# Performance work log

Measured on AMD Instinct MI355X. Metric: run time of the kernel, lower is better.

Reference implementation:

```python
import jax, jax.numpy as jnp
import numpy as np

N_NODES = 100000
N_EDGES = 1200000
IN_DIM = 256
HID = 64


def _spmm(rows, cols, vals, M):
    # sparse (COO) @ dense: gather source rows, scale by edge vals, scatter-add to dest
    gathered = M[cols] * vals[:, None]          # [E, d]
    return jax.ops.segment_sum(gathered, rows, num_segments=N_NODES)


def _gcn_embed(rows, cols, vals, X, W1, b1, W2, b2):
    # layer 1: SELU(A @ (X W1) + b1)
    Z = _spmm(rows, cols, vals, X @ W1) + b1
    Z = jax.nn.selu(Z)
    # layer 2: A @ (Z W2) + b2 (no activation)
    Z = _spmm(rows, cols, vals, Z @ W2) + b2
    # row-wise L2 normalize (F.normalize, p=2, dim=1)
    norm = jnp.sqrt(jnp.sum(Z * Z, axis=1, keepdims=True))
    return Z / jnp.maximum(norm, 1e-12)


def setup_inputs() -> dict:
    key = jax.random.key(0)
    ks = jax.random.split(key, 10)
    X1 = jax.random.normal(ks[0], (N_NODES, IN_DIM), dtype=jnp.float32)
    X2 = jax.random.normal(ks[1], (N_NODES, IN_DIM), dtype=jnp.float32)
    rows1 = jax.random.randint(ks[2], (N_EDGES,), 0, N_NODES, dtype=jnp.int32)
    cols1 = jax.random.randint(ks[3], (N_EDGES,), 0, N_NODES, dtype=jnp.int32)
    vals1 = jax.random.uniform(ks[4], (N_EDGES,), dtype=jnp.float32)
    rows2 = jax.random.randint(ks[5], (N_EDGES,), 0, N_NODES, dtype=jnp.int32)
    cols2 = jax.random.randint(ks[6], (N_EDGES,), 0, N_NODES, dtype=jnp.int32)
    vals2 = jax.random.uniform(ks[7], (N_EDGES,), dtype=jnp.float32)
    # Xavier-uniform weights, zero biases (reset_parameters)
    lim1 = float(np.sqrt(6.0 / (IN_DIM + HID)))
    lim2 = float(np.sqrt(6.0 / (HID + HID)))
    W1 = jax.random.uniform(ks[8], (IN_DIM, HID), dtype=jnp.float32, minval=-lim1, maxval=lim1)
    W2 = jax.random.uniform(ks[9], (HID, HID), dtype=jnp.float32, minval=-lim2, maxval=lim2)
    b1 = jnp.zeros((HID,), dtype=jnp.float32)
    b2 = jnp.zeros((HID,), dtype=jnp.float32)
    return {"X1": X1, "X2": X2, "rows1": rows1, "cols1": cols1, "vals1": vals1,
            "rows2": rows2, "cols2": cols2, "vals2": vals2,
            "W1": W1, "b1": b1, "W2": W2, "b2": b2}


def reference(X1, X2, rows1, cols1, vals1, rows2, cols2, vals2, W1, b1, W2, b2):
    Z1 = _gcn_embed(rows1, cols1, vals1, X1, W1, b1, W2, b2)
    Z2 = _gcn_embed(rows2, cols2, vals2, X2, W1, b1, W2, b2)
    return (Z1, Z2)
```

## Files before the change

### kernel.cpp

```cpp
#include <hip/hip_runtime.h>
#include <hip/hip_bf16.h>


#define RPB 512
#define EPB 4096
#define MAXB 8192

typedef __attribute__((ext_vector_type(8))) short short8;
typedef __attribute__((ext_vector_type(4))) short short4v;
typedef __attribute__((ext_vector_type(4))) float f32x4;

__device__ __forceinline__ float selu_f(float x) {
    const float scale = 1.0507009873554805f;
    const float alpha = 1.6732632423543772f;
    return x > 0.0f ? scale * x : scale * alpha * (__expf(x) - 1.0f);
}

__device__ __forceinline__ short f2bf(float x) {
    unsigned u = __float_as_uint(x);
    u += 0x7FFF + ((u >> 16) & 1);
    return (short)(u >> 16);
}
__device__ __forceinline__ float bf2f(short h) {
    return __uint_as_float(((unsigned)(unsigned short)h) << 16);
}

__global__ void scan_a(const int* __restrict__ countsB, int* __restrict__ offsB,
                       int* __restrict__ partialsB, int N) {
    const int* counts = countsB + (size_t)blockIdx.y * N;
    int* offs = offsB + (size_t)blockIdx.y * (N + 1);
    int* partials = partialsB + (size_t)blockIdx.y * 512;
    __shared__ int sh[256];
    int tid = threadIdx.x;
    int base = blockIdx.x * 1024 + tid * 4;
    int4 c = make_int4(0, 0, 0, 0);
    if (base + 3 < N) {
        c = *(const int4*)(counts + base);
    } else {
        if (base + 0 < N) c.x = counts[base + 0];
        if (base + 1 < N) c.y = counts[base + 1];
        if (base + 2 < N) c.z = counts[base + 2];
        if (base + 3 < N) c.w = counts[base + 3];
    }
    int tsum = c.x + c.y + c.z + c.w;
    sh[tid] = tsum;
    __syncthreads();
    int val = tsum;
    for (int d = 1; d < 256; d <<= 1) {
        int t = (tid >= d) ? sh[tid - d] : 0;
        __syncthreads();
        val += t;
        sh[tid] = val;
        __syncthreads();
    }
    int excl = val - tsum;
    int4 o;
    o.x = excl; o.y = o.x + c.x; o.z = o.y + c.y; o.w = o.z + c.z;
    if (base + 3 < N) {
        *(int4*)(offs + base) = o;
    } else {
        if (base + 0 < N) offs[base + 0] = o.x;
        if (base + 1 < N) offs[base + 1] = o.y;
        if (base + 2 < N) offs[base + 2] = o.z;
        if (base + 3 < N) offs[base + 3] = o.w;
    }
    if (tid == 255) partials[blockIdx.x] = val;
}

__global__ void scan_b(int* __restrict__ partialsB, int nb) {
    int* partials = partialsB + (size_t)blockIdx.y * 512;
    __shared__ int sh[128];
    int tid = threadIdx.x;
    int v = (tid < nb) ? partials[tid] : 0;
    sh[tid] = v;
    __syncthreads();
    int val = v;
    for (int d = 1; d < 128; d <<= 1) {
        int t = (tid >= d) ? sh[tid - d] : 0;
        __syncthreads();
        val += t;
        sh[tid] = val;
        __syncthreads();
    }
    if (tid < nb) partials[tid] = val - v;
}

__global__ void scan_c(int* __restrict__ offsB, const int* __restrict__ partialsB,
                       int N, int E) {
    int* offs = offsB + (size_t)blockIdx.y * (N + 1);
    const int* partials = partialsB + (size_t)blockIdx.y * 512;
    int tid = threadIdx.x;
    int base = blockIdx.x * 1024 + tid * 4;
    int add = partials[blockIdx.x];
    if (base + 3 < N) {
        int4 o = *(int4*)(offs + base);
        o.x += add; o.y += add; o.z += add; o.w += add;
        *(int4*)(offs + base) = o;
    } else {
        for (int t = 0; t < 4; t++)
            if (base + t < N) offs[base + t] += add;
    }
    if (blockIdx.x == 0 && tid == 0) offs[N] = E;
}

__global__ __launch_bounds__(256) void bucket_hist(const int* __restrict__ r0,
                                                   const int* __restrict__ r1,
                                                   int* __restrict__ cntTB,
                                                   int E, int nbA, int NB, int M) {
    const int* rows = blockIdx.y ? r1 : r0;
    int* cntT = cntTB + (size_t)blockIdx.y * M;
    __shared__ int cnt[256];
    int tid = threadIdx.x;
    cnt[tid] = 0;
    __syncthreads();
    int e0 = blockIdx.x * EPB;
#pragma unroll
    for (int k = 0; k < EPB / 256; k++) {
        int e = e0 + k * 256 + tid;
        if (e < E) atomicAdd(&cnt[rows[e] >> 9], 1);
    }
    __syncthreads();
    if (tid < NB) cntT[tid * nbA + blockIdx.x] = cnt[tid];
}

__global__ __launch_bounds__(256) void coarse_scatter(const int* __restrict__ r0,
                                                      const int* __restrict__ r1,
                                                      const int* __restrict__ c0,
                                                      const int* __restrict__ c1,
                                                      const float* __restrict__ v0,
                                                      const float* __restrict__ v1,
                                                      const int* __restrict__ csOffsB,
                                                      int2* __restrict__ ecvAB,
                                                      int E, int nbA, int NB, int M) {
    const int* rows = blockIdx.y ? r1 : r0;
    const int* cols = blockIdx.y ? c1 : c0;
    const float* vals = blockIdx.y ? v1 : v0;
    const int* csOffs = csOffsB + (size_t)blockIdx.y * (M + 1);
    int2* ecvA = ecvAB + (size_t)blockIdx.y * E;
    __shared__ int cnt[256];
    __shared__ int loc[256];
    __shared__ int gof[256];
    __shared__ int dstBase[EPB];
    __shared__ int2 eLDS[EPB];
    int tid = threadIdx.x, blk = blockIdx.x;
    int e0 = blk * EPB;
    cnt[tid] = 0;
    __syncthreads();
#pragma unroll
    for (int k = 0; k < EPB / 256; k++) {
        int e = e0 + k * 256 + tid;
        if (e < E) atomicAdd(&cnt[rows[e] >> 9], 1);
    }
    __syncthreads();
    int my = cnt[tid];
    loc[tid] = my;
    __syncthreads();
    int val = my;
    for (int d = 1; d < 256; d <<= 1) {
        int t = (tid >= d) ? loc[tid - d] : 0;
        __syncthreads();
        val += t;
        loc[tid] = val;
        __syncthreads();
    }
    int excl = val - my;
    loc[tid] = excl;
    cnt[tid] = excl;
    gof[tid] = (tid < NB) ? csOffs[tid * nbA + blk] : 0;
    __syncthreads();
#pragma unroll
    for (int k = 0; k < EPB / 256; k++) {
        int e = e0 + k * 256 + tid;
        if (e < E) {
            int r = rows[e];
            int b = r >> 9;
            int p = atomicAdd(&cnt[b], 1);
            eLDS[p] = make_int2(((r & (RPB - 1)) << 17) | cols[e],
                                __float_as_int(vals[e]));
            dstBase[p] = gof[b] - loc[b];
        }
    }
    __syncthreads();
    int nE = min(EPB, E - e0);
    for (int j = tid; j < nE; j += 256)
        ecvA[dstBase[j] + j] = eLDS[j];
}

__global__ __launch_bounds__(256) void fine_sort(const int* __restrict__ csOffsB,
                                                 const int2* __restrict__ ecvAB,
                                                 int2* __restrict__ ecvB,
                                                 int* __restrict__ offsB,
                                                 int nbA, int N, int E, int M) {
    const int* csOffs = csOffsB + (size_t)blockIdx.y * (M + 1);
    const int2* ecvA = ecvAB + (size_t)blockIdx.y * E;
    int2* ecv = ecvB + (size_t)blockIdx.y * E;
    int* offs = offsB + (size_t)blockIdx.y * (N + 1);
    __shared__ int rcnt[RPB], roff[RPB], rcur[RPB];
    __shared__ int sh[256];
    __shared__ int2 eLDS[MAXB];
    int b = blockIdx.x, tid = threadIdx.x;
    int bs = csOffs[b * nbA];
    int be = csOffs[(b + 1) * nbA];
    int cntE = be - bs;
    if (cntE > MAXB) cntE = MAXB;
    rcnt[tid] = 0;
    rcnt[tid + 256] = 0;
    __syncthreads();
    for (int j = tid; j < cntE; j += 256)
        atomicAdd(&rcnt[ecvA[bs + j].x >> 17], 1);
    __syncthreads();
    int a0 = rcnt[2 * tid], a1 = rcnt[2 * tid + 1];
    int ps = a0 + a1;
    sh[tid] = ps;
    __syncthreads();
    int val = ps;
    for (int d = 1; d < 256; d <<= 1) {
        int t = (tid >= d) ? sh[tid - d] : 0;
        __syncthreads();
        val += t;
        sh[tid] = val;
        __syncthreads();
    }
    int exclPair = val - ps;
    roff[2 * tid] = exclPair;
    roff[2 * tid + 1] = exclPair + a0;
    rcur[2 * tid] = exclPair;
    rcur[2 * tid + 1] = exclPair + a0;
    __syncthreads();
    int row0 = b * RPB;
    for (int t2 = tid; t2 < RPB; t2 += 256) {
        int row = row0 + t2;
        if (row <= N) offs[row] = bs + roff[t2];
    }
    if (b == 0 && tid == 0) offs[N] = E;
    for (int j = tid; j < cntE; j += 256) {
        int2 p = ecvA[bs + j];
        int pos = atomicAdd(&rcur[p.x >> 17], 1);
        if (pos < MAXB) eLDS[pos] = make_int2(p.x & 0x1FFFF, p.y);
    }
    __syncthreads();
    for (int j = tid; j < cntE; j += 256)
        ecv[bs + j] = eLDS[j];
}

__global__ void prep_w2(const float* __restrict__ W1, short* __restrict__ th1,
                        short* __restrict__ tl1,
                        const float* __restrict__ W2, short* __restrict__ th2,
                        short* __restrict__ tl2) {
    int idx = blockIdx.x * 256 + threadIdx.x;
    const int n1 = 256 * 64;
    if (idx < n1) {
        int k = idx >> 6, n = idx & 63;
        float x = W1[idx];
        short h = f2bf(x);
        short l = f2bf(x - bf2f(h));
        th1[n * 256 + k] = h;
        tl1[n * 256 + k] = l;
    } else if (idx - n1 < 64 * 64) {
        int i2 = idx - n1;
        int k = i2 >> 6, n = i2 & 63;
        float x = W2[i2];
        short h = f2bf(x);
        short l = f2bf(x - bf2f(h));
        th2[n * 64 + k] = h;
        tl2[n * 64 + k] = l;
    }
}

template<int K>
__global__ __launch_bounds__(256) void gemm_mfma(const float* __restrict__ A0,
                                                 const float* __restrict__ A1,
                                                 const short* __restrict__ Wth,
                                                 const short* __restrict__ Wtl,
                                                 float* __restrict__ C0,
                                                 float* __restrict__ C1, int M) {
    constexpr int NC = K / 64;
    const float* A = blockIdx.y ? A1 : A0;
    float* C = blockIdx.y ? C1 : C0;
    __shared__ short Ah[64 * 72], Al[64 * 72];
    __shared__ short Wh[64 * 72], Wl[64 * 72];
    int tid = threadIdx.x;
    int wave = tid >> 6, lane = tid & 63;
    int m = lane & 15, q = lane >> 4;
    int row0 = blockIdx.x * 64;
    int ai = tid >> 4;
    int aj = (tid & 15) * 4;
    f32x4 acc[4] = {{0.f, 0.f, 0.f, 0.f}, {0.f, 0.f, 0.f, 0.f},
                    {0.f, 0.f, 0.f, 0.f}, {0.f, 0.f, 0.f, 0.f}};

    float4 ga[4];
#pragma unroll
    for (int v = 0; v < 4; v++) {
        int gr = row0 + v * 16 + ai;
        ga[v] = make_float4(0.f, 0.f, 0.f, 0.f);
        if (gr < M) ga[v] = *(const float4*)(A + (size_t)gr * K + aj);
    }

#pragma unroll
    for (int c = 0; c < NC; c++) {
        short4v whv[4], wlv[4];
#pragma unroll
        for (int v = 0; v < 4; v++) {
            size_t wo = (size_t)(v * 16 + ai) * K + c * 64 + aj;
            whv[v] = *(const short4v*)(Wth + wo);
            wlv[v] = *(const short4v*)(Wtl + wo);
        }
        float4 gan[4];
        if (c + 1 < NC) {
#pragma unroll
            for (int v = 0; v < 4; v++) {
                int gr = row0 + v * 16 + ai;
                gan[v] = make_float4(0.f, 0.f, 0.f, 0.f);
                if (gr < M)
                    gan[v] = *(const float4*)(A + (size_t)gr * K + (c + 1) * 64 + aj);
            }
        }
#pragma unroll
        for (int v = 0; v < 4; v++) {
            int r = v * 16 + ai;
            float f[4] = {ga[v].x, ga[v].y, ga[v].z, ga[v].w};
            short4v h, l;
#pragma unroll
            for (int j = 0; j < 4; j++) {
                short hh = f2bf(f[j]);
                h[j] = hh;
                l[j] = f2bf(f[j] - bf2f(hh));
            }
            *(short4v*)(&Ah[r * 72 + aj]) = h;
            *(short4v*)(&Al[r * 72 + aj]) = l;
        }
#pragma unroll
        for (int v = 0; v < 4; v++) {
            int n = v * 16 + ai;
            *(short4v*)(&Wh[n * 72 + aj]) = whv[v];
            *(short4v*)(&Wl[n * 72 + aj]) = wlv[v];
        }
        __syncthreads();
        int ar = (16 * wave + m) * 72;
        short8 ah0 = *(const short8*)(&Ah[ar + q * 8]);
        short8 ah1 = *(const short8*)(&Ah[ar + 32 + q * 8]);
        short8 al0 = *(const short8*)(&Al[ar + q * 8]);
        short8 al1 = *(const short8*)(&Al[ar + 32 + q * 8]);
#pragma unroll
        for (int nt = 0; nt < 4; nt++) {
            int nb = (nt * 16 + m) * 72;
            short8 bh0 = *(const short8*)(&Wh[nb + q * 8]);
            short8 bh1 = *(const short8*)(&Wh[nb + 32 + q * 8]);
            short8 bl0 = *(const short8*)(&Wl[nb + q * 8]);
            short8 bl1 = *(const short8*)(&Wl[nb + 32 + q * 8]);
            acc[nt] = __builtin_amdgcn_mfma_f32_16x16x32_bf16(ah0, bh0, acc[nt], 0, 0, 0);
            acc[nt] = __builtin_amdgcn_mfma_f32_16x16x32_bf16(al0, bh0, acc[nt], 0, 0, 0);
            acc[nt] = __builtin_amdgcn_mfma_f32_16x16x32_bf16(ah0, bl0, acc[nt], 0, 0, 0);
            acc[nt] = __builtin_amdgcn_mfma_f32_16x16x32_bf16(ah1, bh1, acc[nt], 0, 0, 0);
            acc[nt] = __builtin_amdgcn_mfma_f32_16x16x32_bf16(al1, bh1, acc[nt], 0, 0, 0);
            acc[nt] = __builtin_amdgcn_mfma_f32_16x16x32_bf16(ah1, bl1, acc[nt], 0, 0, 0);
        }
        if (c + 1 < NC) {
            __syncthreads();
#pragma unroll
            for (int v = 0; v < 4; v++) ga[v] = gan[v];
        }
    }
#pragma unroll
    for (int nt = 0; nt < 4; nt++) {
#pragma unroll
        for (int r = 0; r < 4; r++) {
            int grow = row0 + 16 * wave + q * 4 + r;
            if (grow < M) C[(size_t)grow * 64 + nt * 16 + m] = acc[nt][r];
        }
    }
}

__device__ __forceinline__ void spmm_row4(const int* __restrict__ offs,
                                          const int2* __restrict__ ecv,
                                          const float* __restrict__ H,
                                          int row, int g, int f4,
                                          float& ax, float& ay, float& az, float& aw) {
    int s = offs[row], e = offs[row + 1];
    s = __builtin_amdgcn_readfirstlane(s);
    e = __builtin_amdgcn_readfirstlane(e);
    ax = ay = az = aw = 0.f;
    for (int i = s; i < e; i += 8) {
        int i0 = i + g, i1 = i + 4 + g;
        int2 p0 = ecv[i0 < e ? i0 : (e - 1)];
        int2 p1 = ecv[i1 < e ? i1 : (e - 1)];
        float v0 = (i0 < e) ? __int_as_float(p0.y) : 0.f;
        float v1 = (i1 < e) ? __int_as_float(p1.y) : 0.f;
        float4 h0 = *(const float4*)(H + (size_t)p0.x * 64 + f4);
        float4 h1 = *(const float4*)(H + (size_t)p1.x * 64 + f4);
        ax = fmaf(v0, h0.x, ax); ay = fmaf(v0, h0.y, ay);
        az = fmaf(v0, h0.z, az); aw = fmaf(v0, h0.w, aw);
        ax = fmaf(v1, h1.x, ax); ay = fmaf(v1, h1.y, ay);
        az = fmaf(v1, h1.z, az); aw = fmaf(v1, h1.w, aw);
    }
#pragma unroll
    for (int d = 16; d <= 32; d <<= 1) {
        ax += __shfl_xor(ax, d, 64);
        ay += __shfl_xor(ay, d, 64);
        az += __shfl_xor(az, d, 64);
        aw += __shfl_xor(aw, d, 64);
    }
}

__global__ __launch_bounds__(256) void spmm_selu(const int* __restrict__ offsB,
                                                 const int2* __restrict__ ecvB,
                                                 const float* __restrict__ HB,
                                                 const float* __restrict__ bias,
                                                 float* __restrict__ outB,
                                                 int N, int E) {
    int gph = blockIdx.y;
    const int* offs = offsB + (size_t)gph * (N + 1);
    const int2* ecv = ecvB + (size_t)gph * E;
    const float* H = HB + (size_t)gph * N * 64;
    float* out = outB + (size_t)gph * N * 64;
    int row = blockIdx.x * 4 + (threadIdx.x >> 6);
    if (row >= N) return;
    int lane = threadIdx.x & 63;
    int g = lane >> 4, f4 = (lane & 15) * 4;
    float ax, ay, az, aw;
    spmm_row4(offs, ecv, H, row, g, f4, ax, ay, az, aw);
    float4 b = *(const float4*)(bias + f4);
    if (g == 0) {
        float4 o;
        o.x = selu_f(ax + b.x);
        o.y = selu_f(ay + b.y);
        o.z = selu_f(az + b.z);
        o.w = selu_f(aw + b.w);
        *(float4*)(out + (size_t)row * 64 + f4) = o;
    }
}

__global__ __launch_bounds__(256) void spmm_norm(const int* __restrict__ offsB,
                                                 const int2* __restrict__ ecvB,
                                                 const float* __restrict__ HB,
                                                 const float* __restrict__ bias,
                                                 float* __restrict__ outB,
                                                 int N, int E) {
    int gph = blockIdx.y;
    const int* offs = offsB + (size_t)gph * (N + 1);
    const int2* ecv = ecvB + (size_t)gph * E;
    const float* H = HB + (size_t)gph * N * 64;
    float* out = outB + (size_t)gph * N * 64;
    int row = blockIdx.x * 4 + (threadIdx.x >> 6);
    if (row >= N) return;
    int lane = threadIdx.x & 63;
    int g = lane >> 4, f4 = (lane & 15) * 4;
    float ax, ay, az, aw;
    spmm_row4(offs, ecv, H, row, g, f4, ax, ay, az, aw);
    float4 b = *(const float4*)(bias + f4);
    float zx = ax + b.x, zy = ay + b.y, zz = az + b.z, zw = aw + b.w;
    float s2 = zx * zx + zy * zy + zz * zz + zw * zw;
#pragma unroll
    for (int d = 1; d <= 8; d <<= 1) s2 += __shfl_xor(s2, d, 64);
    float inv = 1.0f / fmaxf(sqrtf(s2), 1e-12f);
    if (g == 0) {
        float4 o;
        o.x = zx * inv; o.y = zy * inv; o.z = zz * inv; o.w = zw * inv;
        *(float4*)(out + (size_t)row * 64 + f4) = o;
    }
}

extern "C" void kernel_launch(void* const* d_in, const int* in_sizes, int n_in,
                              void* d_out, int out_size, void* d_ws, size_t ws_size,
                              hipStream_t stream) {
    const int IN_DIM = 256, HID = 64;
    const int N = in_sizes[0] / IN_DIM;
    const int E = in_sizes[2];

    const float* X1 = (const float*)d_in[0];
    const float* X2 = (const float*)d_in[1];
    const int*   r0 = (const int*)d_in[2];
    const int*   c0 = (const int*)d_in[3];
    const float* v0 = (const float*)d_in[4];
    const int*   r1 = (const int*)d_in[5];
    const int*   c1 = (const int*)d_in[6];
    const float* v1 = (const float*)d_in[7];
    const float* W1 = (const float*)d_in[8];
    const float* b1 = (const float*)d_in[9];
    const float* W2 = (const float*)d_in[10];
    const float* b2 = (const float*)d_in[11];
    float* out = (float*)d_out;

    const int NB  = (N + RPB - 1) / RPB;
    const int nbA = (E + EPB - 1) / EPB;
    const int M   = NB * nbA;
    const int nbScanM = (M + 1023) / 1024;
    const int nbGemm = (N + 63) / 64;
    const int nbRow  = (N + 3) / 4;

    auto align16 = [](char* p) { return (char*)(((uintptr_t)p + 15) & ~(uintptr_t)15); };
    char* w = (char*)d_ws;
    float* bufA   = (float*)w; w += (size_t)2 * N * HID * sizeof(float);
    float* bufB   = (float*)w; w += (size_t)2 * N * HID * sizeof(float);
    w = align16(w);
    int2*  ecv    = (int2*)w;  w += (size_t)2 * E * sizeof(int2);
    w = align16(w);
    int*   cntT   = (int*)w;   w += (size_t)2 * M * sizeof(int);
    w = align16(w);
    int*   csOffs = (int*)w;   w += (size_t)2 * (M + 1) * sizeof(int);
    w = align16(w);
    int*   offs   = (int*)w;   w += (size_t)2 * (N + 1) * sizeof(int);
    w = align16(w);
    int*   partials = (int*)w; w += 2 * 512 * sizeof(int);
    w = align16(w);
    short* w1th = (short*)w;   w += (size_t)64 * IN_DIM * sizeof(short);
    short* w1tl = (short*)w;   w += (size_t)64 * IN_DIM * sizeof(short);
    short* w2th = (short*)w;   w += (size_t)64 * HID * sizeof(short);
    short* w2tl = (short*)w;   w += (size_t)64 * HID * sizeof(short);
    int2*  ecvA = (int2*)bufA;

    prep_w2<<<(IN_DIM * 64 + HID * 64 + 255) / 256, 256, 0, stream>>>(
        W1, w1th, w1tl, W2, w2th, w2tl);

    bucket_hist<<<dim3(nbA, 2), 256, 0, stream>>>(r0, r1, cntT, E, nbA, NB, M);
    scan_a<<<dim3(nbScanM, 2), 256, 0, stream>>>(cntT, csOffs, partials, M);
    scan_b<<<dim3(1, 2), 128, 0, stream>>>(partials, nbScanM);
    scan_c<<<dim3(nbScanM, 2), 256, 0, stream>>>(csOffs, partials, M, E);
    coarse_scatter<<<dim3(nbA, 2), 256, 0, stream>>>(r0, r1, c0, c1, v0, v1,
                                                     csOffs, ecvA, E, nbA, NB, M);
    fine_sort<<<dim3(NB, 2), 256, 0, stream>>>(csOffs, ecvA, ecv, offs, nbA, N, E, M);

    gemm_mfma<256><<<dim3(nbGemm, 2), 256, 0, stream>>>(
        X1, X2, w1th, w1tl, bufA, bufA + (size_t)N * HID, N);
    spmm_selu<<<dim3(nbRow, 2), 256, 0, stream>>>(offs, ecv, bufA, b1, bufB, N, E);

    gemm_mfma<64><<<dim3(nbGemm, 2), 256, 0, stream>>>(
        bufB, bufB + (size_t)N * HID, w2th, w2tl, bufA, bufA + (size_t)N * HID, N);
    spmm_norm<<<dim3(nbRow, 2), 256, 0, stream>>>(offs, ecv, bufA, b2, out, N, E);
}
```

Baseline: 537.6 us.

## Fuse layer-1 SpMM+SELU with W2 GEMM via MFMA and unroll gather loop

```diff
diff --git a/kernel.cpp b/kernel.cpp
--- a/kernel.cpp
+++ b/kernel.cpp
@@ -380,18 +380,28 @@
     s = __builtin_amdgcn_readfirstlane(s);
     e = __builtin_amdgcn_readfirstlane(e);
     ax = ay = az = aw = 0.f;
-    for (int i = s; i < e; i += 8) {
-        int i0 = i + g, i1 = i + 4 + g;
+    for (int i = s; i < e; i += 16) {
+        int i0 = i + g, i1 = i + 4 + g, i2 = i + 8 + g, i3 = i + 12 + g;
         int2 p0 = ecv[i0 < e ? i0 : (e - 1)];
         int2 p1 = ecv[i1 < e ? i1 : (e - 1)];
+        int2 p2 = ecv[i2 < e ? i2 : (e - 1)];
+        int2 p3 = ecv[i3 < e ? i3 : (e - 1)];
         float v0 = (i0 < e) ? __int_as_float(p0.y) : 0.f;
         float v1 = (i1 < e) ? __int_as_float(p1.y) : 0.f;
+        float v2 = (i2 < e) ? __int_as_float(p2.y) : 0.f;
+        float v3 = (i3 < e) ? __int_as_float(p3.y) : 0.f;
         float4 h0 = *(const float4*)(H + (size_t)p0.x * 64 + f4);
         float4 h1 = *(const float4*)(H + (size_t)p1.x * 64 + f4);
+        float4 h2 = *(const float4*)(H + (size_t)p2.x * 64 + f4);
+        float4 h3 = *(const float4*)(H + (size_t)p3.x * 64 + f4);
         ax = fmaf(v0, h0.x, ax); ay = fmaf(v0, h0.y, ay);
         az = fmaf(v0, h0.z, az); aw = fmaf(v0, h0.w, aw);
         ax = fmaf(v1, h1.x, ax); ay = fmaf(v1, h1.y, ay);
         az = fmaf(v1, h1.z, az); aw = fmaf(v1, h1.w, aw);
+        ax = fmaf(v2, h2.x, ax); ay = fmaf(v2, h2.y, ay);
+        az = fmaf(v2, h2.z, az); aw = fmaf(v2, h2.w, aw);
+        ax = fmaf(v3, h3.x, ax); ay = fmaf(v3, h3.y, ay);
+        az = fmaf(v3, h3.z, az); aw = fmaf(v3, h3.w, aw);
     }
 #pragma unroll
     for (int d = 16; d <= 32; d <<= 1) {
@@ -402,31 +412,74 @@
     }
 }
 
-__global__ __launch_bounds__(256) void spmm_selu(const int* __restrict__ offsB,
-                                                 const int2* __restrict__ ecvB,
-                                                 const float* __restrict__ HB,
-                                                 const float* __restrict__ bias,
-                                                 float* __restrict__ outB,
-                                                 int N, int E) {
+__global__ __launch_bounds__(256) void spmm_selu_w2(const int* __restrict__ offsB,
+                                                    const int2* __restrict__ ecvB,
+                                                    const float* __restrict__ HB,
+                                                    const float* __restrict__ bias,
+                                                    const short* __restrict__ w2th,
+                                                    const short* __restrict__ w2tl,
+                                                    float* __restrict__ outB,
+                                                    int N, int E) {
     int gph = blockIdx.y;
     const int* offs = offsB + (size_t)gph * (N + 1);
     const int2* ecv = ecvB + (size_t)gph * E;
     const float* H = HB + (size_t)gph * N * 64;
     float* out = outB + (size_t)gph * N * 64;
-    int row = blockIdx.x * 4 + (threadIdx.x >> 6);
-    if (row >= N) return;
-    int lane = threadIdx.x & 63;
+    __shared__ short Zh[16 * 72], Zl[16 * 72];
+    int tid = threadIdx.x, wave = tid >> 6, lane = tid & 63;
     int g = lane >> 4, f4 = (lane & 15) * 4;
-    float ax, ay, az, aw;
-    spmm_row4(offs, ecv, H, row, g, f4, ax, ay, az, aw);
+    int rbase = blockIdx.x * 16;
     float4 b = *(const float4*)(bias + f4);
-    if (g == 0) {
-        float4 o;
-        o.x = selu_f(ax + b.x);
-        o.y = selu_f(ay + b.y);
-        o.z = selu_f(az + b.z);
-        o.w = selu_f(aw + b.w);
-        *(float4*)(out + (size_t)row * 64 + f4) = o;
+#pragma unroll
+    for (int rr = 0; rr < 4; rr++) {
+        int lr = wave * 4 + rr;
+        int row = rbase + lr;
+        if (row < N) {
+            float ax, ay, az, aw;
+            spmm_row4(offs, ecv, H, row, g, f4, ax, ay, az, aw);
+            if (g == 0) {
+                float zx = selu_f(ax + b.x);
+                float zy = selu_f(ay + b.y);
+                float zz = selu_f(az + b.z);
+                float zw = selu_f(aw + b.w);
+                short4v h, l;
+                h.x = f2bf(zx); l.x = f2bf(zx - bf2f(h.x));
+                h.y = f2bf(zy); l.y = f2bf(zy - bf2f(h.y));
+                h.z = f2bf(zz); l.z = f2bf(zz - bf2f(h.z));
+                h.w = f2bf(zw); l.w = f2bf(zw - bf2f(h.w));
+                *(short4v*)(&Zh[lr * 72 + f4]) = h;
+                *(short4v*)(&Zl[lr * 72 + f4]) = l;
+            }
+        } else if (g == 0) {
+            short4v zv = {0, 0, 0, 0};
+            *(short4v*)(&Zh[lr * 72 + f4]) = zv;
+            *(short4v*)(&Zl[lr * 72 + f4]) = zv;
+        }
+    }
+    __syncthreads();
+    int m_ = lane & 15, q = lane >> 4;
+    int ar = m_ * 72;
+    short8 ah0 = *(const short8*)(&Zh[ar + q * 8]);
+    short8 ah1 = *(const short8*)(&Zh[ar + 32 + q * 8]);
+    short8 al0 = *(const short8*)(&Zl[ar + q * 8]);
+    short8 al1 = *(const short8*)(&Zl[ar + 32 + q * 8]);
+    const short* bhp = w2th + (size_t)(wave * 16 + m_) * 64;
+    const short* blp = w2tl + (size_t)(wave * 16 + m_) * 64;
+    short8 bh0 = *(const short8*)(bhp + q * 8);
+    short8 bh1 = *(const short8*)(bhp + 32 + q * 8);
+    short8 bl0 = *(const short8*)(blp + q * 8);
+    short8 bl1 = *(const short8*)(blp + 32 + q * 8);
+    f32x4 acc = {0.f, 0.f, 0.f, 0.f};
+    acc = __builtin_amdgcn_mfma_f32_16x16x32_bf16(ah0, bh0, acc, 0, 0, 0);
+    acc = __builtin_amdgcn_mfma_f32_16x16x32_bf16(al0, bh0, acc, 0, 0, 0);
+    acc = __builtin_amdgcn_mfma_f32_16x16x32_bf16(ah0, bl0, acc, 0, 0, 0);
+    acc = __builtin_amdgcn_mfma_f32_16x16x32_bf16(ah1, bh1, acc, 0, 0, 0);
+    acc = __builtin_amdgcn_mfma_f32_16x16x32_bf16(al1, bh1, acc, 0, 0, 0);
+    acc = __builtin_amdgcn_mfma_f32_16x16x32_bf16(ah1, bl1, acc, 0, 0, 0);
+#pragma unroll
+    for (int r = 0; r < 4; r++) {
+        int grow = rbase + q * 4 + r;
+        if (grow < N) out[(size_t)grow * 64 + wave * 16 + m_] = acc[r];
     }
 }
 
@@ -487,6 +540,7 @@
     const int nbScanM = (M + 1023) / 1024;
     const int nbGemm = (N + 63) / 64;
     const int nbRow  = (N + 3) / 4;
+    const int nbFuse = (N + 15) / 16;
 
     auto align16 = [](char* p) { return (char*)(((uintptr_t)p + 15) & ~(uintptr_t)15); };
     char* w = (char*)d_ws;
@@ -522,9 +576,7 @@
 
     gemm_mfma<256><<<dim3(nbGemm, 2), 256, 0, stream>>>(
         X1, X2, w1th, w1tl, bufA, bufA + (size_t)N * HID, N);
-    spmm_selu<<<dim3(nbRow, 2), 256, 0, stream>>>(offs, ecv, bufA, b1, bufB, N, E);
-
-    gemm_mfma<64><<<dim3(nbGemm, 2), 256, 0, stream>>>(
-        bufB, bufB + (size_t)N * HID, w2th, w2tl, bufA, bufA + (size_t)N * HID, N);
-    spmm_norm<<<dim3(nbRow, 2), 256, 0, stream>>>(offs, ecv, bufA, b2, out, N, E);
-}
+    spmm_selu_w2<<<dim3(nbFuse, 2), 256, 0, stream>>>(offs, ecv, bufA, b1,
+                                                      w2th, w2tl, bufB, N, E);
+    spmm_norm<<<dim3(nbRow, 2), 256, 0, stream>>>(offs, ecv, bufB, b2, out, N, E);
+}
```

New measurement: 520.2 us. -3.2%, faster.
